# Optimization experiments

Hardware: AMD Instinct MI355X
Metric: run time of the kernel (lower is better)

Reference implementation:

```python
import jax, jax.numpy as jnp
import numpy as np

N_NODES = 50000
N_EDGES = 800000
N_GRAPHS = 512
IN_C, HID, OUT_C = 128, 256, 16


def _mlp(h, w1, b1, w2, b2):
    # PyG-style 2-layer MLP: Linear -> ReLU -> Linear (plain last layer)
    return jax.nn.relu(h @ w1 + b1) @ w2 + b2


def setup_inputs() -> dict:
    key = jax.random.key(0)
    ks = jax.random.split(key, 16)
    x = jax.random.normal(ks[0], (N_NODES, IN_C), dtype=jnp.float32)
    edge_index = jax.random.randint(ks[1], (2, N_EDGES), 0, N_NODES, dtype=jnp.int64)
    batch = jnp.sort(jax.random.randint(ks[2], (N_NODES,), 0, N_GRAPHS, dtype=jnp.int64))

    def lin(k, fan_in, fan_out):
        s = 1.0 / np.sqrt(fan_in)
        return jax.random.uniform(k, (fan_in, fan_out), jnp.float32, -s, s)

    inp = {"x": x, "edge_index": edge_index, "batch": batch}
    dims = [(IN_C, HID), (HID, HID), (HID, HID)]
    ki = 3
    for li, (din, dh) in enumerate(dims):
        inp[f"c{li}_w1"] = lin(ks[ki], din, dh); ki += 1
        inp[f"c{li}_b1"] = jnp.zeros((dh,), jnp.float32)
        inp[f"c{li}_w2"] = lin(ks[ki], dh, dh); ki += 1
        inp[f"c{li}_b2"] = jnp.zeros((dh,), jnp.float32)
    inp["out_w1"] = lin(ks[ki], HID, HID); ki += 1
    inp["out_b1"] = jnp.zeros((HID,), jnp.float32)
    inp["out_w2"] = lin(ks[ki], HID, OUT_C); ki += 1
    inp["out_b2"] = jnp.zeros((OUT_C,), jnp.float32)
    return inp


def reference(x, edge_index, batch,
              c0_w1, c0_b1, c0_w2, c0_b2,
              c1_w1, c1_b1, c1_w2, c1_b2,
              c2_w1, c2_b1, c2_w2, c2_b2,
              out_w1, out_b1, out_w2, out_b2):
    src, dst = edge_index[0], edge_index[1]
    params = [(c0_w1, c0_b1, c0_w2, c0_b2),
              (c1_w1, c1_b1, c1_w2, c1_b2),
              (c2_w1, c2_b1, c2_w2, c2_b2)]
    h = x
    for (w1, b1, w2, b2) in params:
        # GINConv with eps=0: MLP(x + sum_{j in N(i)} x_j)
        agg = jax.ops.segment_sum(h[src], dst, num_segments=N_NODES)
        h = _mlp(h + agg, w1, b1, w2, b2)
        h = jax.nn.relu(h)
        # dropout: identity (eval mode)
    # global mean pool over graphs
    sums = jax.ops.segment_sum(h, batch, num_segments=N_GRAPHS)
    counts = jax.ops.segment_sum(jnp.ones((N_NODES,), h.dtype), batch, num_segments=N_GRAPHS)
    pooled = sums / jnp.maximum(counts, 1.0)[:, None]
    return _mlp(pooled, out_w1, out_b1, out_w2, out_b2)
```

## Files before the change

kernel.cpp:

```cpp
#include <hip/hip_runtime.h>

#define N_NODES 50000
#define N_EDGES 800000
#define N_GRAPHS 512
#define IN_C 128
#define HID 256
#define OUT_C 16

typedef __attribute__((ext_vector_type(8))) short short8;
typedef __attribute__((ext_vector_type(4))) float f32x4;

__device__ __forceinline__ float bf2f(unsigned short u) {
    return __uint_as_float(((unsigned int)u) << 16);
}
__device__ __forceinline__ unsigned short f2bf(float f) {
    unsigned int u = __float_as_uint(f);
    u += 0x7fff + ((u >> 16) & 1);
    return (unsigned short)(u >> 16);
}

#define PLANE_ELEMS ((long)N_NODES * 32)

struct PrepArgs {
    const float* x;
    const float* w[6];
    ushort* xbf;
    ushort* wt[6];
    int* deg;
    float* sums;
};

__global__ __launch_bounds__(256) void prep_kernel(PrepArgs a) {
    const int X4    = N_NODES * IN_C / 4;
    const int TW    = IN_C * HID;
    const int TH    = HID * HID;
    const int TBASE = X4;
    const int TEND  = TBASE + TW + 5 * TH;
    const int D4    = N_NODES / 4;
    const int DBASE = TEND;
    const int SBASE = DBASE + D4;
    const int S4    = N_GRAPHS * HID / 4;
    const long total = (long)SBASE + S4;

    long stride = (long)gridDim.x * blockDim.x;
    for (long i = (long)blockIdx.x * blockDim.x + threadIdx.x; i < total; i += stride) {
        if (i < X4) {
            float4 v = ((const float4*)a.x)[i];
            ushort4 o;
            o.x = f2bf(v.x); o.y = f2bf(v.y); o.z = f2bf(v.z); o.w = f2bf(v.w);
            long e = i * 4;
            int node = (int)(e >> 7);
            int col  = (int)(e & 127);
            long off = (long)(col >> 5) * PLANE_ELEMS + (long)node * 32 + (col & 31);
            *(ushort4*)(a.xbf + off) = o;
        } else if (i < TEND) {
            long r = i - TBASE;
            int wi, shift;
            long off;
            if (r < TW) { wi = 0; shift = 7; off = r; }
            else { r -= TW; wi = 1 + (int)(r / TH); shift = 8; off = r % TH; }
            int n = (int)(off >> shift);
            int k = (int)(off - ((long)n << shift));
            a.wt[wi][off] = f2bf(a.w[wi][(long)k * HID + n]);
        } else if (i < SBASE) {
            ((int4*)a.deg)[i - DBASE] = make_int4(0, 0, 0, 0);
        } else {
            ((float4*)a.sums)[i - SBASE] = make_float4(0.f, 0.f, 0.f, 0.f);
        }
    }
}

__global__ void deg_kernel(const int* __restrict__ dst, int* __restrict__ deg) {
    int e = blockIdx.x * blockDim.x + threadIdx.x;
    if (e < N_EDGES) atomicAdd(&deg[dst[e]], 1);
}

__global__ __launch_bounds__(256) void scan_block(const int* __restrict__ deg,
                                                  int* __restrict__ partial,
                                                  int* __restrict__ blockSums) {
    __shared__ int s[256];
    int t = threadIdx.x;
    int i = blockIdx.x * 256 + t;
    int v = (i < N_NODES) ? deg[i] : 0;
    s[t] = v;
    __syncthreads();
    #pragma unroll
    for (int off = 1; off < 256; off <<= 1) {
        int add = (t >= off) ? s[t - off] : 0;
        __syncthreads();
        s[t] += add;
        __syncthreads();
    }
    if (i < N_NODES) partial[i] = s[t] - v;
    if (t == 255) blockSums[blockIdx.x] = s[255];
}

__global__ __launch_bounds__(256) void add_offsets_fused(
    const int* __restrict__ partial, const int* __restrict__ blockSums,
    int* __restrict__ rowptr, int* __restrict__ cursor, int nb) {
    __shared__ int s[256];
    __shared__ int myOff;
    int t = threadIdx.x;
    int v = (t < nb) ? blockSums[t] : 0;
    s[t] = v;
    __syncthreads();
    #pragma unroll
    for (int off = 1; off < 256; off <<= 1) {
        int add = (t >= off) ? s[t - off] : 0;
        __syncthreads();
        s[t] += add;
        __syncthreads();
    }
    if (t == blockIdx.x) myOff = s[t] - v;
    __syncthreads();
    int i = blockIdx.x * 256 + t;
    if (i < N_NODES) {
        int r = partial[i] + myOff;
        rowptr[i] = r;
        cursor[i] = r;
    }
    if (i == 0) rowptr[N_NODES] = N_EDGES;
}

__global__ void bucket_edges(const int* __restrict__ src, const int* __restrict__ dst,
                             int* __restrict__ cursor, int* __restrict__ srcSorted) {
    int e = blockIdx.x * blockDim.x + threadIdx.x;
    if (e >= N_EDGES) return;
    int p = atomicAdd(&cursor[dst[e]], 1);
    __builtin_nontemporal_store(src[e], &srcSorted[p]);
}

template <int C>
__global__ __launch_bounds__(256) void gin_aggregate_planar(
    const ushort* __restrict__ hp,
    const int* __restrict__ rowptr,
    const int* __restrict__ srcIdx,
    ushort* __restrict__ out)
{
    constexpr int NC  = C / 32;
    constexpr int PER = 8 / NC;

    int b  = blockIdx.x;
    int x8 = b & 7;
    int chunk   = x8 / PER;
    int nodeblk = (b >> 3) * PER + (x8 & (PER - 1));

    int lane = threadIdx.x & 63;
    int wave = threadIdx.x >> 6;
    int grp  = lane >> 2;
    int l    = lane & 3;
    int node = nodeblk * 64 + wave * 16 + grp;
    if (node >= N_NODES) return;

    const ushort* plane = hp + (long)chunk * PLANE_ELEMS + l * 8;

    float acc[8];
    {
        short8 sv = *(const short8*)(plane + (long)node * 32);
        #pragma unroll
        for (int v = 0; v < 8; ++v) acc[v] = bf2f((unsigned short)sv[v]);
    }

    int beg = rowptr[node], end = rowptr[node + 1];
    int k = beg;
    for (; k + 8 <= end; k += 8) {
        int si[8];
        #pragma unroll
        for (int u = 0; u < 8; ++u) si[u] = srcIdx[k + u];
        short8 r[8];
        #pragma unroll
        for (int u = 0; u < 8; ++u) r[u] = *(const short8*)(plane + (long)si[u] * 32);
        #pragma unroll
        for (int u = 0; u < 8; ++u)
            #pragma unroll
            for (int v = 0; v < 8; ++v) acc[v] += bf2f((unsigned short)r[u][v]);
    }
    for (; k + 2 <= end; k += 2) {
        int si0 = srcIdx[k], si1 = srcIdx[k + 1];
        short8 r0 = *(const short8*)(plane + (long)si0 * 32);
        short8 r1 = *(const short8*)(plane + (long)si1 * 32);
        #pragma unroll
        for (int v = 0; v < 8; ++v) acc[v] += bf2f((unsigned short)r0[v]);
        #pragma unroll
        for (int v = 0; v < 8; ++v) acc[v] += bf2f((unsigned short)r1[v]);
    }
    if (k < end) {
        short8 r = *(const short8*)(plane + (long)srcIdx[k] * 32);
        #pragma unroll
        for (int v = 0; v < 8; ++v) acc[v] += bf2f((unsigned short)r[v]);
    }

    short8 o;
    #pragma unroll
    for (int v = 0; v < 8; ++v) o[v] = (short)f2bf(acc[v]);
    __builtin_nontemporal_store(o, (short8*)(out + (long)node * C + chunk * 32 + l * 8));
}

template <int K1, bool FUSE_POOL>
__global__ __launch_bounds__(512, 2) void gin_mlp_persist(
    const ushort* __restrict__ A,
    const ushort* __restrict__ w1t,
    const float* __restrict__ b1,
    const ushort* __restrict__ w2t,
    const float* __restrict__ b2,
    ushort* __restrict__ out,
    const int* __restrict__ batch,
    float* __restrict__ sums,
    int M, int nTiles, int nPers)
{
    constexpr int NCH1 = K1 / 8;
    constexpr int NSLOT1 = 64 * NCH1;
    constexpr int NS1 = K1 / 32;
    constexpr int PFN = NSLOT1 / 512;

    __shared__ short LsA[NSLOT1 * 8];
    __shared__ short LsH[2048 * 8];

    int t = threadIdx.x;
    int lane = t & 63;
    int wv = t >> 6;
    int quad = lane >> 4;
    int l15 = lane & 15;
    int swz = l15 & 7;
    int col0 = wv * 32;

    short8 w1r[NS1 * 2];
    #pragma unroll
    for (int s = 0; s < NS1; ++s)
        #pragma unroll
        for (int j = 0; j < 2; ++j)
            w1r[s * 2 + j] = *(const short8*)(w1t + (long)(col0 + j * 16 + l15) * K1 + s * 32 + quad * 8);
    short8 w2r[16];
    #pragma unroll
    for (int s = 0; s < 8; ++s)
        #pragma unroll
        for (int j = 0; j < 2; ++j)
            w2r[s * 2 + j] = *(const short8*)(w2t + (long)(col0 + j * 16 + l15) * 256 + s * 32 + quad * 8);
    float bv1[2], bv2[2];
    #pragma unroll
    for (int j = 0; j < 2; ++j) {
        bv1[j] = b1[col0 + j * 16 + l15];
        bv2[j] = b2[col0 + j * 16 + l15];
    }

    int t0 = (int)(((long)blockIdx.x * nTiles) / nPers);
    int t1 = (int)(((long)(blockIdx.x + 1) * nTiles) / nPers);

    const f32x4 zero = {0.f, 0.f, 0.f, 0.f};

    for (int ti = t0; ti < t1; ++ti) {
        int row0 = ti * 64;

        #pragma unroll
        for (int c = 0; c < PFN; ++c) {
            int s = c * 512 + t;
            int row = s / NCH1;
            int kcs = s & (NCH1 - 1);
            int kc = kcs ^ (row & 7);
            int grow = row0 + row;
            if (grow >= M) grow = M - 1;
            *(short8*)&LsA[s * 8] = *(const short8*)(A + (long)grow * K1 + kc * 8);
        }
        __syncthreads();

        f32x4 acc[4][2];
        #pragma unroll
        for (int i = 0; i < 4; ++i)
            #pragma unroll
            for (int j = 0; j < 2; ++j) acc[i][j] = zero;

        #pragma unroll
        for (int s = 0; s < NS1; ++s) {
            #pragma unroll
            for (int i = 0; i < 4; ++i) {
                int row = i * 16 + l15;
                int slot = row * NCH1 + ((s * 4 + quad) ^ swz);
                short8 a = *(const short8*)&LsA[slot * 8];
                acc[i][0] = __builtin_amdgcn_mfma_f32_16x16x32_bf16(a, w1r[s * 2 + 0], acc[i][0], 0, 0, 0);
                acc[i][1] = __builtin_amdgcn_mfma_f32_16x16x32_bf16(a, w1r[s * 2 + 1], acc[i][1], 0, 0, 0);
            }
        }
        __syncthreads();

        #pragma unroll
        for (int i = 0; i < 4; ++i)
            #pragma unroll
            for (int j = 0; j < 2; ++j) {
                int col = col0 + j * 16 + l15;
                int kc2 = col >> 3, sub = col & 7;
                #pragma unroll
                for (int r = 0; r < 4; ++r) {
                    int row = i * 16 + quad * 4 + r;
                    int slot = row * 32 + (kc2 ^ (row & 7));
                    float o = fmaxf(acc[i][j][r] + bv1[j], 0.f);
                    LsH[slot * 8 + sub] = (short)f2bf(o);
                }
            }
        __syncthreads();

        #pragma unroll
        for (int i = 0; i < 4; ++i)
            #pragma unroll
            for (int j = 0; j < 2; ++j) acc[i][j] = zero;

        #pragma unroll
        for (int s = 0; s < 8; ++s) {
            #pragma unroll
            for (int i = 0; i < 4; ++i) {
                int row = i * 16 + l15;
                int slot = row * 32 + ((s * 4 + quad) ^ swz);
                short8 a = *(const short8*)&LsH[slot * 8];
                acc[i][0] = __builtin_amdgcn_mfma_f32_16x16x32_bf16(a, w2r[s * 2 + 0], acc[i][0], 0, 0, 0);
                acc[i][1] = __builtin_amdgcn_mfma_f32_16x16x32_bf16(a, w2r[s * 2 + 1], acc[i][1], 0, 0, 0);
            }
        }

        if constexpr (!FUSE_POOL) {
            #pragma unroll
            for (int i = 0; i < 4; ++i)
                #pragma unroll
                for (int r = 0; r < 4; ++r) {
                    int grow = row0 + i * 16 + quad * 4 + r;
                    if (grow >= M) continue;
                    #pragma unroll
                    for (int j = 0; j < 2; ++j) {
                        int col = col0 + j * 16 + l15;
                        float o = fmaxf(acc[i][j][r] + bv2[j], 0.f);
                        out[(long)(col >> 5) * PLANE_ELEMS + (long)grow * 32 + (col & 31)] = f2bf(o);
                    }
                }
        } else {
            float pacc[2];
            #pragma unroll
            for (int j = 0; j < 2; ++j) pacc[j] = 0.f;
            int cur = -1;
            #pragma unroll
            for (int i = 0; i < 4; ++i) {
                #pragma unroll
                for (int r = 0; r < 4; ++r) {
                    int row = row0 + i * 16 + quad * 4 + r;
                    if (row >= M) continue;
                    int g = batch[row];
                    if (g != cur) {
                        if (cur >= 0) {
                            #pragma unroll
                            for (int j = 0; j < 2; ++j)
                                atomicAdd(&sums[(long)cur * 256 + col0 + j * 16 + l15], pacc[j]);
                        }
                        cur = g;
                        #pragma unroll
                        for (int j = 0; j < 2; ++j) pacc[j] = 0.f;
                    }
                    #pragma unroll
                    for (int j = 0; j < 2; ++j)
                        pacc[j] += fmaxf(acc[i][j][r] + bv2[j], 0.f);
                }
            }
            if (cur >= 0) {
                #pragma unroll
                for (int j = 0; j < 2; ++j)
                    atomicAdd(&sums[(long)cur * 256 + col0 + j * 16 + l15], pacc[j]);
            }
        }
    }
}

__global__ __launch_bounds__(256) void final_mlp_kernel(
    const float* __restrict__ sums, const int* __restrict__ batch,
    const float* __restrict__ w1, const float* __restrict__ b1,
    const float* __restrict__ w2, const float* __restrict__ b2,
    float* __restrict__ out) {
    __shared__ float row[HID];
    __shared__ float hid[HID];
    __shared__ int cntS;
    int g = blockIdx.x;
    int t = threadIdx.x;
    if (t == 0) {
        int lo = 0, hi = N_NODES;
        while (lo < hi) { int m = (lo + hi) >> 1; if (batch[m] < g) lo = m + 1; else hi = m; }
        int lo2 = lo, hi2 = N_NODES;
        while (lo2 < hi2) { int m = (lo2 + hi2) >> 1; if (batch[m] < g + 1) lo2 = m + 1; else hi2 = m; }
        cntS = lo2 - lo;
    }
    __syncthreads();
    float cnt = fmaxf((float)cntS, 1.0f);
    row[t] = sums[(long)g * HID + t] / cnt;
    __syncthreads();
    float acc = b1[t];
    for (int k = 0; k < HID; ++k) acc += row[k] * w1[k * HID + t];
    hid[t] = fmaxf(acc, 0.f);
    __syncthreads();
    if (t < OUT_C) {
        float o = b2[t];
        for (int k = 0; k < HID; ++k) o += hid[k] * w2[k * OUT_C + t];
        out[(long)g * OUT_C + t] = o;
    }
}

extern "C" void kernel_launch(void* const* d_in, const int* in_sizes, int n_in,
                              void* d_out, int out_size, void* d_ws, size_t ws_size,
                              hipStream_t stream) {
    const float* x     = (const float*)d_in[0];
    const int*   ei    = (const int*)d_in[1];
    const int*   batch = (const int*)d_in[2];
    const int*   src   = ei;
    const int*   dst   = ei + N_EDGES;

    const float* c_w1[3] = { (const float*)d_in[3],  (const float*)d_in[7],  (const float*)d_in[11] };
    const float* c_b1[3] = { (const float*)d_in[4],  (const float*)d_in[8],  (const float*)d_in[12] };
    const float* c_w2[3] = { (const float*)d_in[5],  (const float*)d_in[9],  (const float*)d_in[13] };
    const float* c_b2[3] = { (const float*)d_in[6],  (const float*)d_in[10], (const float*)d_in[14] };
    const float* out_w1 = (const float*)d_in[15];
    const float* out_b1 = (const float*)d_in[16];
    const float* out_w2 = (const float*)d_in[17];
    const float* out_b2 = (const float*)d_in[18];

    char* p = (char*)d_ws;
    auto alloc = [&](size_t bytes) {
        char* r = p;
        p += (bytes + 15) & ~(size_t)15;
        return r;
    };
    ushort* xbf  = (ushort*)alloc((size_t)N_NODES * IN_C * 2);
    ushort* bufA = (ushort*)alloc((size_t)N_NODES * HID * 2);
    ushort* bufB = (ushort*)alloc((size_t)N_NODES * HID * 2);
    ushort* wt[6];
    wt[0] = (ushort*)alloc((size_t)IN_C * HID * 2);
    for (int i = 1; i < 6; ++i) wt[i] = (ushort*)alloc((size_t)HID * HID * 2);
    float* sums   = (float*)alloc((size_t)N_GRAPHS * HID * 4);
    int* deg       = (int*)alloc((size_t)N_NODES * 4);
    int* rowptr    = (int*)alloc((size_t)(N_NODES + 1) * 4);
    int* blockSums = (int*)alloc(256 * 4);
    int* cursor    = (int*)alloc((size_t)N_NODES * 4);
    int* srcSorted = (int*)alloc((size_t)N_EDGES * 4);

    const int nb = (N_NODES + 255) / 256;

    {
        PrepArgs a;
        a.x = x;
        a.w[0] = c_w1[0]; a.w[1] = c_w2[0];
        a.w[2] = c_w1[1]; a.w[3] = c_w2[1];
        a.w[4] = c_w1[2]; a.w[5] = c_w2[2];
        a.xbf = xbf;
        for (int i = 0; i < 6; ++i) a.wt[i] = wt[i];
        a.deg = deg;
        a.sums = sums;
        prep_kernel<<<2048, 256, 0, stream>>>(a);
    }

    deg_kernel<<<(N_EDGES + 255) / 256, 256, 0, stream>>>(dst, deg);
    scan_block<<<nb, 256, 0, stream>>>(deg, rowptr, blockSums);
    add_offsets_fused<<<nb, 256, 0, stream>>>(rowptr, blockSums, rowptr, cursor, nb);
    bucket_edges<<<(N_EDGES + 255) / 256, 256, 0, stream>>>(src, dst, cursor, srcSorted);

    const int nodeBlks = (N_NODES + 63) / 64;
    const int aggX128  = nodeBlks * (IN_C / 32);
    const int aggX256  = nodeBlks * (HID / 32);
    const int NPERS    = 256;

    gin_aggregate_planar<IN_C><<<aggX128, 256, 0, stream>>>(xbf, rowptr, srcSorted, bufB);
    gin_mlp_persist<IN_C, false><<<NPERS, 512, 0, stream>>>(bufB, wt[0], c_b1[0], wt[1], c_b2[0],
                                                            bufA, batch, sums, N_NODES, nodeBlks, NPERS);

    gin_aggregate_planar<HID><<<aggX256, 256, 0, stream>>>(bufA, rowptr, srcSorted, bufB);
    gin_mlp_persist<HID, false><<<NPERS, 512, 0, stream>>>(bufB, wt[2], c_b1[1], wt[3], c_b2[1],
                                                           bufA, batch, sums, N_NODES, nodeBlks, NPERS);

    gin_aggregate_planar<HID><<<aggX256, 256, 0, stream>>>(bufA, rowptr, srcSorted, bufB);
    gin_mlp_persist<HID, true><<<NPERS, 512, 0, stream>>>(bufB, wt[4], c_b1[2], wt[5], c_b2[2],
                                                          bufA, batch, sums, N_NODES, nodeBlks, NPERS);

    final_mlp_kernel<<<N_GRAPHS, 256, 0, stream>>>(sums, batch, out_w1, out_b1,
                                                   out_w2, out_b2, (float*)d_out);
}
```

Before: 432.7 us.

## Record per-edge rank in degree pass and scatter edges without atomics, sharded by destination

The degree-count kernel now saves the return value of each atomicAdd as the edge's rank within its destination. The bucketing pass drops its second round of atomics and writes each edge to rowptr[d]+rank[e]. That scatter is split into 8 destination shards, with block index low bits choosing the shard, probably to keep each XCD's writes within a narrower address range for cache locality. In exchange it stores an extra 3.2MB rank array, and every shard block rereads dst for all edges in its chunk, so dst reads rise about eightfold.

```diff
diff --git a/kernel.cpp b/kernel.cpp
--- a/kernel.cpp
+++ b/kernel.cpp
@@ -70,9 +70,10 @@
     }
 }
 
-__global__ void deg_kernel(const int* __restrict__ dst, int* __restrict__ deg) {
+__global__ void deg_rank_kernel(const int* __restrict__ dst, int* __restrict__ deg,
+                                int* __restrict__ rank) {
     int e = blockIdx.x * blockDim.x + threadIdx.x;
-    if (e < N_EDGES) atomicAdd(&deg[dst[e]], 1);
+    if (e < N_EDGES) rank[e] = atomicAdd(&deg[dst[e]], 1);
 }
 
 __global__ __launch_bounds__(256) void scan_block(const int* __restrict__ deg,
@@ -97,7 +98,7 @@
 
 __global__ __launch_bounds__(256) void add_offsets_fused(
     const int* __restrict__ partial, const int* __restrict__ blockSums,
-    int* __restrict__ rowptr, int* __restrict__ cursor, int nb) {
+    int* __restrict__ rowptr, int nb) {
     __shared__ int s[256];
     __shared__ int myOff;
     int t = threadIdx.x;
@@ -114,20 +115,33 @@
     if (t == blockIdx.x) myOff = s[t] - v;
     __syncthreads();
     int i = blockIdx.x * 256 + t;
-    if (i < N_NODES) {
-        int r = partial[i] + myOff;
-        rowptr[i] = r;
-        cursor[i] = r;
-    }
+    if (i < N_NODES) rowptr[i] = partial[i] + myOff;
     if (i == 0) rowptr[N_NODES] = N_EDGES;
 }
 
-__global__ void bucket_edges(const int* __restrict__ src, const int* __restrict__ dst,
-                             int* __restrict__ cursor, int* __restrict__ srcSorted) {
-    int e = blockIdx.x * blockDim.x + threadIdx.x;
-    if (e >= N_EDGES) return;
-    int p = atomicAdd(&cursor[dst[e]], 1);
-    __builtin_nontemporal_store(src[e], &srcSorted[p]);
+#define NSHARD 8
+#define SHARD_SZ ((N_NODES + NSHARD - 1) / NSHARD)
+#define EDGES_PER_BLK 2048
+
+__global__ __launch_bounds__(256) void scatter_edges_sharded(
+    const int* __restrict__ src, const int* __restrict__ dst,
+    const int* __restrict__ rank, const int* __restrict__ rowptr,
+    int* __restrict__ srcSorted) {
+    int b = blockIdx.x;
+    int shard = b & 7;
+    int chunk = b >> 3;
+    int lo = shard * SHARD_SZ;
+    int hi = lo + SHARD_SZ;
+    int base = chunk * EDGES_PER_BLK + threadIdx.x;
+    #pragma unroll
+    for (int u = 0; u < EDGES_PER_BLK / 256; ++u) {
+        int e = base + u * 256;
+        if (e < N_EDGES) {
+            int d = dst[e];
+            if (d >= lo && d < hi)
+                srcSorted[rowptr[d] + rank[e]] = src[e];
+        }
+    }
 }
 
 template <int C>
@@ -431,7 +445,7 @@
     int* deg       = (int*)alloc((size_t)N_NODES * 4);
     int* rowptr    = (int*)alloc((size_t)(N_NODES + 1) * 4);
     int* blockSums = (int*)alloc(256 * 4);
-    int* cursor    = (int*)alloc((size_t)N_NODES * 4);
+    int* rank      = (int*)alloc((size_t)N_EDGES * 4);
     int* srcSorted = (int*)alloc((size_t)N_EDGES * 4);
 
     const int nb = (N_NODES + 255) / 256;
@@ -449,10 +463,13 @@
         prep_kernel<<<2048, 256, 0, stream>>>(a);
     }
 
-    deg_kernel<<<(N_EDGES + 255) / 256, 256, 0, stream>>>(dst, deg);
+    deg_rank_kernel<<<(N_EDGES + 255) / 256, 256, 0, stream>>>(dst, deg, rank);
     scan_block<<<nb, 256, 0, stream>>>(deg, rowptr, blockSums);
-    add_offsets_fused<<<nb, 256, 0, stream>>>(rowptr, blockSums, rowptr, cursor, nb);
-    bucket_edges<<<(N_EDGES + 255) / 256, 256, 0, stream>>>(src, dst, cursor, srcSorted);
+    add_offsets_fused<<<nb, 256, 0, stream>>>(rowptr, blockSums, rowptr, nb);
+    {
+        const int chunks = (N_EDGES + EDGES_PER_BLK - 1) / EDGES_PER_BLK;
+        scatter_edges_sharded<<<chunks * NSHARD, 256, 0, stream>>>(src, dst, rank, rowptr, srcSorted);
+    }
 
     const int nodeBlks = (N_NODES + 63) / 64;
     const int aggX128  = nodeBlks * (IN_C / 32);
```

Result: faster. 397.0 us (-8.2%).
